# Optimization experiments

Measured on AMD Instinct MI355X. Metric: run time of the kernel, lower is better.

Reference implementation:

```python
import jax, jax.numpy as jnp
import numpy as np

D_MODEL, D_K, D_V = 1024, 64, 64
B, S = 4, 4096


def setup_inputs() -> dict:
    key = jax.random.key(0)
    ks = jax.random.split(key, 13)
    s = 1.0 / np.sqrt(D_MODEL)
    inp = {
        "q": jax.random.normal(ks[0], (B, S, D_MODEL), jnp.float32),
        "k": jax.random.normal(ks[1], (B, S, D_MODEL), jnp.float32),
        "v": jax.random.normal(ks[2], (B, S, D_MODEL), jnp.float32),
        "mask": jax.random.randint(ks[3], (1, S, S), 0, 2, jnp.int32),
        "Wq": jax.random.normal(ks[4], (D_K, D_MODEL), jnp.float32) * s,
        "bq": jax.random.normal(ks[5], (D_K,), jnp.float32) * s,
        "Wk": jax.random.normal(ks[6], (D_K, D_MODEL), jnp.float32) * s,
        "bk": jax.random.normal(ks[7], (D_K,), jnp.float32) * s,
        "Wv": jax.random.normal(ks[8], (D_V, D_MODEL), jnp.float32) * s,
        "bv": jax.random.normal(ks[9], (D_V,), jnp.float32) * s,
        "Wo": jax.random.normal(ks[10], (D_MODEL, D_V), jnp.float32) / np.sqrt(D_V),
        "bo": jax.random.normal(ks[11], (D_MODEL,), jnp.float32) / np.sqrt(D_V),
    }
    return inp


def reference(q, k, v, mask, Wq, bq, Wk, bk, Wv, bv, Wo, bo):
    # linear projections (torch Linear: x @ W.T + b)
    qh = jnp.einsum("bsd,kd->bsk", q, Wq) + bq   # [B,S,d_k]
    kh = jnp.einsum("bsd,kd->bsk", k, Wk) + bk   # [B,S,d_k]
    vh = jnp.einsum("bsd,vd->bsv", v, Wv) + bv   # [B,S,d_v]
    scale = 1.0 / jnp.sqrt(jnp.float32(D_K))
    scores = jnp.einsum("bqk,bmk->bqm", qh, kh) * scale  # [B,S,S]
    scores = jnp.where(mask == 0, jnp.float32(-1e9), scores)
    attn = jax.nn.softmax(scores, axis=-1)
    out = jnp.einsum("bqm,bmv->bqv", attn, vh)   # [B,S,d_v]
    return jnp.einsum("bqv,dv->bqd", out, Wo) + bo
```

## Files before the change

### kernel.cpp

```cpp
#include <hip/hip_runtime.h>
#include <cmath>

typedef __attribute__((ext_vector_type(8))) short bf16x8;
typedef __attribute__((ext_vector_type(4))) short bf16x4;
typedef __attribute__((ext_vector_type(4))) float f32x4;

constexpr int B_ = 4;
constexpr int S_ = 4096;
constexpr int DM_ = 1024;
constexpr int DK_ = 64;
constexpr int NROW = B_ * S_;

__device__ __forceinline__ short f2bf(float x) {
  union { float f; unsigned u; } c; c.f = x;
  unsigned r = (c.u + 0x7FFF + ((c.u >> 16) & 1)) >> 16;
  return (short)r;
}
__device__ __forceinline__ float bf2f(short h) {
  union { float f; unsigned u; } c; c.u = ((unsigned)(unsigned short)h) << 16;
  return c.f;
}

__global__ __launch_bounds__(256) void maskpack(
    const int* __restrict__ mask, unsigned long long* __restrict__ bits) {
  const int wid = (blockIdx.x * 256 + threadIdx.x) >> 6;
  const int lane = threadIdx.x & 63;
  const size_t base = (size_t)wid * 4096;
  for (int it = 0; it < 64; ++it) {
    int m = mask[base + it * 64 + lane];
    unsigned long long b = __ballot(m != 0);
    if (lane == 0) bits[(size_t)wid * 64 + it] = b;
  }
}

__global__ __launch_bounds__(256) void proj_mfma(
    const float* __restrict__ q, const float* __restrict__ k,
    const float* __restrict__ v,
    const float* __restrict__ Wq, const float* __restrict__ bq,
    const float* __restrict__ Wk, const float* __restrict__ bk,
    const float* __restrict__ Wv, const float* __restrict__ bv,
    short* __restrict__ qh, short* __restrict__ kh, short* __restrict__ vhT) {
  const int mat = blockIdx.z;
  const float* X    = mat == 0 ? q  : (mat == 1 ? k  : v);
  const float* W    = mat == 0 ? Wq : (mat == 1 ? Wk : Wv);
  const float* bias = mat == 0 ? bq : (mat == 1 ? bk : bv);

  __shared__ float Xs[128][68];
  __shared__ short Ws[64][72];

  const int t = threadIdx.x;
  const int row0 = blockIdx.x * 128;
  const int lane = t & 63, w = t >> 6, quad = lane >> 4, l16 = lane & 15;

  f32x4 acc[2][4] = {};

  for (int k0 = 0; k0 < DM_; k0 += 64) {
    __syncthreads();
    {
      const int rr = t >> 3, cc = (t & 7) * 8;
#pragma unroll
      for (int pass = 0; pass < 4; ++pass) {
        int r = pass * 32 + rr;
        const float* src = X + (size_t)(row0 + r) * DM_ + k0 + cc;
        *(f32x4*)&Xs[r][cc]     = *(const f32x4*)src;
        *(f32x4*)&Xs[r][cc + 4] = *(const f32x4*)(src + 4);
      }
    }
    {
      int c = t >> 2, kk = (t & 3) * 16;
      const float* src = W + (size_t)c * DM_ + k0 + kk;
      f32x4 a0 = *(const f32x4*)src, a1 = *(const f32x4*)(src + 4);
      f32x4 a2 = *(const f32x4*)(src + 8), a3 = *(const f32x4*)(src + 12);
      bf16x8 w0, w1;
#pragma unroll
      for (int j = 0; j < 4; ++j) {
        w0[j] = f2bf(a0[j]); w0[j + 4] = f2bf(a1[j]);
        w1[j] = f2bf(a2[j]); w1[j + 4] = f2bf(a3[j]);
      }
      *(bf16x8*)&Ws[c][kk]     = w0;
      *(bf16x8*)&Ws[c][kk + 8] = w1;
    }
    __syncthreads();

#pragma unroll
    for (int c = 0; c < 2; ++c) {
      bf16x8 bw[4];
#pragma unroll
      for (int ct = 0; ct < 4; ++ct)
        bw[ct] = *(const bf16x8*)&Ws[16 * ct + l16][c * 32 + quad * 8];
#pragma unroll
      for (int rt = 0; rt < 2; ++rt) {
        const float* xp = &Xs[32 * w + 16 * rt + l16][c * 32 + quad * 8];
        f32x4 x0 = *(const f32x4*)xp;
        f32x4 x1 = *(const f32x4*)(xp + 4);
        bf16x8 ahi, alo;
#pragma unroll
        for (int j = 0; j < 4; ++j) {
          short h0 = f2bf(x0[j]); ahi[j] = h0;     alo[j]     = f2bf(x0[j] - bf2f(h0));
          short h1 = f2bf(x1[j]); ahi[j + 4] = h1; alo[j + 4] = f2bf(x1[j] - bf2f(h1));
        }
#pragma unroll
        for (int ct = 0; ct < 4; ++ct) {
          acc[rt][ct] = __builtin_amdgcn_mfma_f32_16x16x32_bf16(ahi, bw[ct], acc[rt][ct], 0, 0, 0);
          acc[rt][ct] = __builtin_amdgcn_mfma_f32_16x16x32_bf16(alo, bw[ct], acc[rt][ct], 0, 0, 0);
        }
      }
    }
  }

  float bs[4];
#pragma unroll
  for (int ct = 0; ct < 4; ++ct) bs[ct] = bias[16 * ct + l16];

  short* dstq = (mat == 0) ? qh : kh;
#pragma unroll
  for (int rt = 0; rt < 2; ++rt)
#pragma unroll
    for (int ct = 0; ct < 4; ++ct)
#pragma unroll
      for (int reg = 0; reg < 4; ++reg) {
        int r = row0 + 32 * w + 16 * rt + quad * 4 + reg;
        int c = 16 * ct + l16;
        short hv = f2bf(acc[rt][ct][reg] + bs[ct]);
        if (mat == 2)
          vhT[((size_t)(r >> 12) * DK_ + c) * S_ + (r & 4095)] = hv;
        else
          dstq[(size_t)r * DK_ + c] = hv;
      }
}

__global__ __launch_bounds__(256) void attn_mfma(
    const short* __restrict__ qh, const short* __restrict__ kh,
    const short* __restrict__ vhT, const unsigned int* __restrict__ mbits,
    float* __restrict__ Opart, float* __restrict__ mpart,
    float* __restrict__ lpart, int ns) {
  __shared__ short ks[64][72];
  __shared__ short vt[64][72];
  __shared__ short ps[4][16][72];

  const int b = blockIdx.z;
  const int split = blockIdx.y;
  const int q0 = blockIdx.x * 64;
  const int t = threadIdx.x, lane = t & 63, w = t >> 6;
  const int quad = lane >> 4, l16 = lane & 15;
  const int myq = q0 + 16 * w + l16;

  const int kt0 = split * (S_ / ns);
  const int kt1 = kt0 + S_ / ns;

  bf16x8 qf[2];
  {
    const short* src = qh + ((size_t)b * S_ + myq) * DK_ + quad * 8;
    qf[0] = *(const bf16x8*)src;
    qf[1] = *(const bf16x8*)(src + 32);
  }

  f32x4 ao[4] = {};
  float m_i = -INFINITY, l_i = 0.0f;

  const int sr = t >> 2;
  const int sseg = t & 3;

  for (int kt = kt0; kt < kt1; kt += 64) {
    __syncthreads();
    {
      const short* srck = kh + ((size_t)b * S_ + kt + sr) * DK_;
      *(bf16x8*)&ks[sr][8 * sseg]       = *(const bf16x8*)(srck + 8 * sseg);
      *(bf16x8*)&ks[sr][8 * (sseg + 4)] = *(const bf16x8*)(srck + 8 * (sseg + 4));
      const short* srcv = vhT + ((size_t)b * DK_ + sr) * S_ + kt;
      *(bf16x8*)&vt[sr][8 * sseg]       = *(const bf16x8*)(srcv + 8 * sseg);
      *(bf16x8*)&vt[sr][8 * (sseg + 4)] = *(const bf16x8*)(srcv + 8 * (sseg + 4));
    }
    const uint2 mw = *(const uint2*)&mbits[(size_t)myq * 128 + (kt >> 5)];
    __syncthreads();

    f32x4 sacc[4] = {};
#pragma unroll
    for (int c = 0; c < 2; ++c)
#pragma unroll
      for (int tt = 0; tt < 4; ++tt) {
        bf16x8 a = *(const bf16x8*)&ks[16 * tt + l16][c * 32 + quad * 8];
        sacc[tt] = __builtin_amdgcn_mfma_f32_16x16x32_bf16(a, qf[c], sacc[tt], 0, 0, 0);
      }

    float sc[16];
#pragma unroll
    for (int tt = 0; tt < 4; ++tt) {
      unsigned wrd = (tt & 2) ? mw.y : mw.x;
      int base = (tt & 1) * 16 + quad * 4;
#pragma unroll
      for (int r = 0; r < 4; ++r)
        sc[tt * 4 + r] = ((wrd >> (base + r)) & 1) ? sacc[tt][r] * 0.125f : -1e9f;
    }

    float mx = sc[0];
#pragma unroll
    for (int i = 1; i < 16; ++i) mx = fmaxf(mx, sc[i]);
    mx = fmaxf(mx, __shfl_xor(mx, 16));
    mx = fmaxf(mx, __shfl_xor(mx, 32));
    float m_new = fmaxf(m_i, mx);
    float alpha = __expf(m_i - m_new);
    float p[16], sum = 0.0f;
#pragma unroll
    for (int i = 0; i < 16; ++i) { p[i] = __expf(sc[i] - m_new); sum += p[i]; }
    sum += __shfl_xor(sum, 16);
    sum += __shfl_xor(sum, 32);
    l_i = l_i * alpha + sum;
    m_i = m_new;

#pragma unroll
    for (int tt = 0; tt < 4; ++tt) {
      bf16x4 pk;
#pragma unroll
      for (int r = 0; r < 4; ++r) pk[r] = f2bf(p[tt * 4 + r]);
      *(bf16x4*)&ps[w][l16][16 * tt + quad * 4] = pk;
    }

#pragma unroll
    for (int dt = 0; dt < 4; ++dt)
#pragma unroll
      for (int r = 0; r < 4; ++r) ao[dt][r] *= alpha;

#pragma unroll
    for (int c = 0; c < 2; ++c) {
      bf16x8 bp = *(const bf16x8*)&ps[w][l16][c * 32 + quad * 8];
#pragma unroll
      for (int dt = 0; dt < 4; ++dt) {
        bf16x8 av = *(const bf16x8*)&vt[16 * dt + l16][c * 32 + quad * 8];
        ao[dt] = __builtin_amdgcn_mfma_f32_16x16x32_bf16(av, bp, ao[dt], 0, 0, 0);
      }
    }
  }

  const size_t prow = (size_t)split * NROW + (size_t)b * S_ + myq;
#pragma unroll
  for (int dt = 0; dt < 4; ++dt)
    *(f32x4*)&Opart[prow * DK_ + 16 * dt + quad * 4] = ao[dt];
  if (quad == 0) {
    mpart[prow] = m_i;
    lpart[prow] = l_i;
  }
}

__global__ __launch_bounds__(256) void attn_combine(
    const float* __restrict__ Opart, const float* __restrict__ mpart,
    const float* __restrict__ lpart, short* __restrict__ o_bf, int ns) {
  const int t = threadIdx.x;
  const int row = blockIdx.x * 64 + (t >> 2);
  const int c0 = (t & 3) * 16;

  float M = -INFINITY;
  for (int s = 0; s < ns; ++s) M = fmaxf(M, mpart[(size_t)s * NROW + row]);
  float L = 0.0f, wt[4];
  for (int s = 0; s < ns; ++s) {
    wt[s] = __expf(mpart[(size_t)s * NROW + row] - M);
    L += wt[s] * lpart[(size_t)s * NROW + row];
  }
  float acc[16] = {};
  for (int s = 0; s < ns; ++s) {
    const float* src = Opart + ((size_t)s * NROW + row) * DK_ + c0;
#pragma unroll
    for (int j = 0; j < 16; j += 4) {
      f32x4 vv = *(const f32x4*)(src + j);
#pragma unroll
      for (int r = 0; r < 4; ++r) acc[j + r] += wt[s] * vv[r];
    }
  }
  const float inv = 1.0f / L;
  bf16x8 o0, o1;
#pragma unroll
  for (int j = 0; j < 8; ++j) {
    o0[j] = f2bf(acc[j] * inv);
    o1[j] = f2bf(acc[j + 8] * inv);
  }
  *(bf16x8*)&o_bf[(size_t)row * DK_ + c0]     = o0;
  *(bf16x8*)&o_bf[(size_t)row * DK_ + c0 + 8] = o1;
}

__global__ __launch_bounds__(256) void outproj_mfma(
    const short* __restrict__ o_bf, const float* __restrict__ Wo,
    const float* __restrict__ bo, float* __restrict__ out) {
  __shared__ short os[64][72];
  __shared__ short wos[256][72];

  const int t = threadIdx.x, lane = t & 63, w = t >> 6;
  const int quad = lane >> 4, l16 = lane & 15;
  const int s0 = blockIdx.y * 64;
  const int dm0 = blockIdx.x * 256;

  {
    int r = t >> 2, cq = (t & 3) * 16;
    const short* src = o_bf + (size_t)(s0 + r) * DK_ + cq;
    *(bf16x8*)&os[r][cq]     = *(const bf16x8*)src;
    *(bf16x8*)&os[r][cq + 8] = *(const bf16x8*)(src + 8);
  }
#pragma unroll
  for (int pass = 0; pass < 4; ++pass) {
    int r = pass * 64 + (t >> 2), cq = (t & 3) * 16;
    const float* src = Wo + (size_t)(dm0 + r) * DK_ + cq;
    f32x4 a0 = *(const f32x4*)src, a1 = *(const f32x4*)(src + 4);
    f32x4 a2 = *(const f32x4*)(src + 8), a3 = *(const f32x4*)(src + 12);
    bf16x8 v0, v1;
#pragma unroll
    for (int j = 0; j < 4; ++j) {
      v0[j] = f2bf(a0[j]); v0[j + 4] = f2bf(a1[j]);
      v1[j] = f2bf(a2[j]); v1[j + 4] = f2bf(a3[j]);
    }
    *(bf16x8*)&wos[r][cq]     = v0;
    *(bf16x8*)&wos[r][cq + 8] = v1;
  }
  __syncthreads();

  bf16x8 af[2];
#pragma unroll
  for (int c = 0; c < 2; ++c)
    af[c] = *(const bf16x8*)&os[16 * w + l16][c * 32 + quad * 8];

  f32x4 acc[16] = {};
#pragma unroll
  for (int c = 0; c < 2; ++c)
#pragma unroll
    for (int nt = 0; nt < 16; ++nt) {
      bf16x8 bw = *(const bf16x8*)&wos[16 * nt + l16][c * 32 + quad * 8];
      acc[nt] = __builtin_amdgcn_mfma_f32_16x16x32_bf16(af[c], bw, acc[nt], 0, 0, 0);
    }

  float bias_r[16];
#pragma unroll
  for (int nt = 0; nt < 16; ++nt) bias_r[nt] = bo[dm0 + 16 * nt + l16];

#pragma unroll
  for (int nt = 0; nt < 16; ++nt)
#pragma unroll
    for (int reg = 0; reg < 4; ++reg) {
      int s = s0 + 16 * w + quad * 4 + reg;
      int dm = dm0 + 16 * nt + l16;
      out[(size_t)s * DM_ + dm] = acc[nt][reg] + bias_r[nt];
    }
}

extern "C" void kernel_launch(void* const* d_in, const int* in_sizes, int n_in,
                              void* d_out, int out_size, void* d_ws,
                              size_t ws_size, hipStream_t stream) {
  (void)in_sizes; (void)n_in; (void)out_size;
  const float* q  = (const float*)d_in[0];
  const float* k  = (const float*)d_in[1];
  const float* v  = (const float*)d_in[2];
  const int* mask = (const int*)d_in[3];
  const float* Wq = (const float*)d_in[4];
  const float* bq = (const float*)d_in[5];
  const float* Wk = (const float*)d_in[6];
  const float* bk = (const float*)d_in[7];
  const float* Wv = (const float*)d_in[8];
  const float* bv = (const float*)d_in[9];
  const float* Wo = (const float*)d_in[10];
  const float* bo = (const float*)d_in[11];
  float* out = (float*)d_out;

  short* qh  = (short*)d_ws;
  short* kh  = qh + (size_t)NROW * DK_;
  short* vhT = kh + (size_t)NROW * DK_;
  unsigned int* mbits = (unsigned int*)(vhT + (size_t)NROW * DK_);
  short* o_bf = (short*)(mbits + (size_t)S_ * 128);
  float* mpart = (float*)(o_bf + (size_t)NROW * DK_);
  float* lpart = mpart + 4 * NROW;
  float* Opart = lpart + 4 * NROW;

  const size_t base_bytes = (size_t)((char*)Opart - (char*)d_ws);
  const size_t per_split = (size_t)NROW * DK_ * sizeof(float);
  int ns = 1;
  if (ws_size >= base_bytes + 4 * per_split) ns = 4;
  else if (ws_size >= base_bytes + 2 * per_split) ns = 2;

  maskpack<<<1024, 256, 0, stream>>>(mask, (unsigned long long*)mbits);
  proj_mfma<<<dim3(NROW / 128, 1, 3), 256, 0, stream>>>(
      q, k, v, Wq, bq, Wk, bk, Wv, bv, qh, kh, vhT);
  attn_mfma<<<dim3(S_ / 64, ns, B_), 256, 0, stream>>>(
      qh, kh, vhT, mbits, Opart, mpart, lpart, ns);
  attn_combine<<<NROW / 64, 256, 0, stream>>>(Opart, mpart, lpart, o_bf, ns);
  outproj_mfma<<<dim3(DM_ / 256, NROW / 64), 256, 0, stream>>>(o_bf, Wo, bo, out);
}
```

Measured before the change: 387.6 us.

## Fuse mask packing into projection kernel, halve projection tiles, allow eight KV splits

Mask bit-packing moves out of its own kernel and runs as a fourth z-slice of the projection kernel, which saves one launch and lets the mask read overlap with the projection GEMMs. The projection tile shrinks from 128 to 64 rows per block. This doubles the block count, and the hi/lo bf16 split of X is now done once at staging into shared memory rather than per MFMA read. The attention split count can now rise to 8 when the workspace allows, which adds parallelism but costs more partial-result traffic in the combine step.

```diff
diff --git a/kernel.cpp b/kernel.cpp
--- a/kernel.cpp
+++ b/kernel.cpp
@@ -19,18 +19,6 @@
 __device__ __forceinline__ float bf2f(short h) {
   union { float f; unsigned u; } c; c.u = ((unsigned)(unsigned short)h) << 16;
   return c.f;
-}
-
-__global__ __launch_bounds__(256) void maskpack(
-    const int* __restrict__ mask, unsigned long long* __restrict__ bits) {
-  const int wid = (blockIdx.x * 256 + threadIdx.x) >> 6;
-  const int lane = threadIdx.x & 63;
-  const size_t base = (size_t)wid * 4096;
-  for (int it = 0; it < 64; ++it) {
-    int m = mask[base + it * 64 + lane];
-    unsigned long long b = __ballot(m != 0);
-    if (lane == 0) bits[(size_t)wid * 64 + it] = b;
-  }
 }
 
 __global__ __launch_bounds__(256) void proj_mfma(
@@ -39,35 +27,61 @@
     const float* __restrict__ Wq, const float* __restrict__ bq,
     const float* __restrict__ Wk, const float* __restrict__ bk,
     const float* __restrict__ Wv, const float* __restrict__ bv,
-    short* __restrict__ qh, short* __restrict__ kh, short* __restrict__ vhT) {
+    short* __restrict__ qh, short* __restrict__ kh, short* __restrict__ vhT,
+    const int* __restrict__ mask, unsigned long long* __restrict__ mbits) {
   const int mat = blockIdx.z;
+  const int t = threadIdx.x;
+  const int lane = t & 63, w = t >> 6;
+
+  if (mat == 3) {
+    const int wid = blockIdx.x * 4 + w;
+#pragma unroll
+    for (int j = 0; j < 4; ++j) {
+      const int row = wid + j * 1024;
+      const size_t base = (size_t)row * S_;
+      for (int it = 0; it < 64; ++it) {
+        int m = mask[base + it * 64 + lane];
+        unsigned long long b = __ballot(m != 0);
+        if (lane == 0) mbits[(size_t)row * 64 + it] = b;
+      }
+    }
+    return;
+  }
+
   const float* X    = mat == 0 ? q  : (mat == 1 ? k  : v);
   const float* W    = mat == 0 ? Wq : (mat == 1 ? Wk : Wv);
   const float* bias = mat == 0 ? bq : (mat == 1 ? bk : bv);
 
-  __shared__ float Xs[128][68];
+  __shared__ short Xh[64][72];
+  __shared__ short Xl[64][72];
   __shared__ short Ws[64][72];
 
-  const int t = threadIdx.x;
-  const int row0 = blockIdx.x * 128;
-  const int lane = t & 63, w = t >> 6, quad = lane >> 4, l16 = lane & 15;
-
-  f32x4 acc[2][4] = {};
+  const int row0 = blockIdx.x * 64;
+  const int quad = lane >> 4, l16 = lane & 15;
+
+  f32x4 acc[4] = {};
 
   for (int k0 = 0; k0 < DM_; k0 += 64) {
     __syncthreads();
     {
-      const int rr = t >> 3, cc = (t & 7) * 8;
-#pragma unroll
-      for (int pass = 0; pass < 4; ++pass) {
-        int r = pass * 32 + rr;
-        const float* src = X + (size_t)(row0 + r) * DM_ + k0 + cc;
-        *(f32x4*)&Xs[r][cc]     = *(const f32x4*)src;
-        *(f32x4*)&Xs[r][cc + 4] = *(const f32x4*)(src + 4);
-      }
+      const int r = t >> 2, cq = (t & 3) * 16;
+      const float* src = X + (size_t)(row0 + r) * DM_ + k0 + cq;
+      f32x4 a0 = *(const f32x4*)src, a1 = *(const f32x4*)(src + 4);
+      f32x4 a2 = *(const f32x4*)(src + 8), a3 = *(const f32x4*)(src + 12);
+      bf16x8 h0, h1, l0, l1;
+#pragma unroll
+      for (int j = 0; j < 4; ++j) {
+        short h;
+        h = f2bf(a0[j]); h0[j] = h;     l0[j]     = f2bf(a0[j] - bf2f(h));
+        h = f2bf(a1[j]); h0[j + 4] = h; l0[j + 4] = f2bf(a1[j] - bf2f(h));
+        h = f2bf(a2[j]); h1[j] = h;     l1[j]     = f2bf(a2[j] - bf2f(h));
+        h = f2bf(a3[j]); h1[j + 4] = h; l1[j + 4] = f2bf(a3[j] - bf2f(h));
+      }
+      *(bf16x8*)&Xh[r][cq] = h0; *(bf16x8*)&Xh[r][cq + 8] = h1;
+      *(bf16x8*)&Xl[r][cq] = l0; *(bf16x8*)&Xl[r][cq + 8] = l1;
     }
     {
-      int c = t >> 2, kk = (t & 3) * 16;
+      const int c = t >> 2, kk = (t & 3) * 16;
       const float* src = W + (size_t)c * DM_ + k0 + kk;
       f32x4 a0 = *(const f32x4*)src, a1 = *(const f32x4*)(src + 4);
       f32x4 a2 = *(const f32x4*)(src + 8), a3 = *(const f32x4*)(src + 12);
@@ -84,49 +98,32 @@
 
 #pragma unroll
     for (int c = 0; c < 2; ++c) {
-      bf16x8 bw[4];
-#pragma unroll
-      for (int ct = 0; ct < 4; ++ct)
-        bw[ct] = *(const bf16x8*)&Ws[16 * ct + l16][c * 32 + quad * 8];
-#pragma unroll
-      for (int rt = 0; rt < 2; ++rt) {
-        const float* xp = &Xs[32 * w + 16 * rt + l16][c * 32 + quad * 8];
-        f32x4 x0 = *(const f32x4*)xp;
-        f32x4 x1 = *(const f32x4*)(xp + 4);
-        bf16x8 ahi, alo;
-#pragma unroll
-        for (int j = 0; j < 4; ++j) {
-          short h0 = f2bf(x0[j]); ahi[j] = h0;     alo[j]     = f2bf(x0[j] - bf2f(h0));
-          short h1 = f2bf(x1[j]); ahi[j + 4] = h1; alo[j + 4] = f2bf(x1[j] - bf2f(h1));
-        }
-#pragma unroll
-        for (int ct = 0; ct < 4; ++ct) {
-          acc[rt][ct] = __builtin_amdgcn_mfma_f32_16x16x32_bf16(ahi, bw[ct], acc[rt][ct], 0, 0, 0);
-          acc[rt][ct] = __builtin_amdgcn_mfma_f32_16x16x32_bf16(alo, bw[ct], acc[rt][ct], 0, 0, 0);
-        }
-      }
-    }
-  }
-
-  float bs[4];
-#pragma unroll
-  for (int ct = 0; ct < 4; ++ct) bs[ct] = bias[16 * ct + l16];
+      bf16x8 ahi = *(const bf16x8*)&Xh[16 * w + l16][c * 32 + quad * 8];
+      bf16x8 alo = *(const bf16x8*)&Xl[16 * w + l16][c * 32 + quad * 8];
+#pragma unroll
+      for (int ct = 0; ct < 4; ++ct) {
+        bf16x8 bw = *(const bf16x8*)&Ws[16 * ct + l16][c * 32 + quad * 8];
+        acc[ct] = __builtin_amdgcn_mfma_f32_16x16x32_bf16(ahi, bw, acc[ct], 0, 0, 0);
+        acc[ct] = __builtin_amdgcn_mfma_f32_16x16x32_bf16(alo, bw, acc[ct], 0, 0, 0);
+      }
+    }
+  }
 
   short* dstq = (mat == 0) ? qh : kh;
 #pragma unroll
-  for (int rt = 0; rt < 2; ++rt)
-#pragma unroll
-    for (int ct = 0; ct < 4; ++ct)
-#pragma unroll
-      for (int reg = 0; reg < 4; ++reg) {
-        int r = row0 + 32 * w + 16 * rt + quad * 4 + reg;
-        int c = 16 * ct + l16;
-        short hv = f2bf(acc[rt][ct][reg] + bs[ct]);
-        if (mat == 2)
-          vhT[((size_t)(r >> 12) * DK_ + c) * S_ + (r & 4095)] = hv;
-        else
-          dstq[(size_t)r * DK_ + c] = hv;
-      }
+  for (int ct = 0; ct < 4; ++ct) {
+    const float bs = bias[16 * ct + l16];
+#pragma unroll
+    for (int reg = 0; reg < 4; ++reg) {
+      int r = row0 + 16 * w + quad * 4 + reg;
+      int c = 16 * ct + l16;
+      short hv = f2bf(acc[ct][reg] + bs);
+      if (mat == 2)
+        vhT[((size_t)(r >> 12) * DK_ + c) * S_ + (r & 4095)] = hv;
+      else
+        dstq[(size_t)r * DK_ + c] = hv;
+    }
+  }
 }
 
 __global__ __launch_bounds__(256) void attn_mfma(
@@ -251,7 +248,7 @@
 
   float M = -INFINITY;
   for (int s = 0; s < ns; ++s) M = fmaxf(M, mpart[(size_t)s * NROW + row]);
-  float L = 0.0f, wt[4];
+  float L = 0.0f, wt[8];
   for (int s = 0; s < ns; ++s) {
     wt[s] = __expf(mpart[(size_t)s * NROW + row] - M);
     L += wt[s] * lpart[(size_t)s * NROW + row];
@@ -363,18 +360,19 @@
   unsigned int* mbits = (unsigned int*)(vhT + (size_t)NROW * DK_);
   short* o_bf = (short*)(mbits + (size_t)S_ * 128);
   float* mpart = (float*)(o_bf + (size_t)NROW * DK_);
-  float* lpart = mpart + 4 * NROW;
-  float* Opart = lpart + 4 * NROW;
+  float* lpart = mpart + 8 * NROW;
+  float* Opart = lpart + 8 * NROW;
 
   const size_t base_bytes = (size_t)((char*)Opart - (char*)d_ws);
   const size_t per_split = (size_t)NROW * DK_ * sizeof(float);
   int ns = 1;
-  if (ws_size >= base_bytes + 4 * per_split) ns = 4;
+  if (ws_size >= base_bytes + 8 * per_split) ns = 8;
+  else if (ws_size >= base_bytes + 4 * per_split) ns = 4;
   else if (ws_size >= base_bytes + 2 * per_split) ns = 2;
 
-  maskpack<<<1024, 256, 0, stream>>>(mask, (unsigned long long*)mbits);
-  proj_mfma<<<dim3(NROW / 128, 1, 3), 256, 0, stream>>>(
-      q, k, v, Wq, bq, Wk, bk, Wv, bv, qh, kh, vhT);
+  proj_mfma<<<dim3(NROW / 64, 1, 4), 256, 0, stream>>>(
+      q, k, v, Wq, bq, Wk, bk, Wv, bv, qh, kh, vhT,
+      mask, (unsigned long long*)mbits);
   attn_mfma<<<dim3(S_ / 64, ns, B_), 256, 0, stream>>>(
       qh, kh, vhT, mbits, Opart, mpart, lpart, ns);
   attn_combine<<<NROW / 64, 256, 0, stream>>>(Opart, mpart, lpart, o_bf, ns);
```

Result: slower. 429.5 us (+10.8%).
